# Kernel optimization log

Hardware: AMD Instinct MI355X
Metric: run time of the kernel (lower is better)

Reference implementation:

```python
import jax, jax.numpy as jnp
import numpy as np

B = 16384
D = 1024          # fusion_hidden == depth_hidden == expert hidden
ORD_H = 512       # max(48, fusion_hidden // 2)
E = 7             # num_size_classes (= number of depth experts)
C_SIZE = 7        # num_size_classes
C_DEPTH = 3       # num_depth_classes


def _lin(key, fan_in, fan_out):
    return jax.random.normal(key, (fan_in, fan_out), dtype=jnp.float32) / np.sqrt(fan_in)


def setup_inputs() -> dict:
    key = jax.random.key(0)
    ks = jax.random.split(key, 16)
    inp = {
        'hybrid_feat': jax.random.normal(ks[0], (B, D), dtype=jnp.float32),
        # size_cls_head: Linear(D, D) -> ReLU -> Linear(D, 7)
        'Wc1': _lin(ks[1], D, D), 'bc1': jnp.zeros((D,), jnp.float32),
        'Wc2': _lin(ks[2], D, C_SIZE), 'bc2': jnp.zeros((C_SIZE,), jnp.float32),
        # size_ord_head: Linear(D, 512) -> ReLU -> Linear(512, 6)
        'Wo1': _lin(ks[3], D, ORD_H), 'bo1': jnp.zeros((ORD_H,), jnp.float32),
        'Wo2': _lin(ks[4], ORD_H, C_SIZE - 1), 'bo2': jnp.zeros((C_SIZE - 1,), jnp.float32),
        # size_residual_head: Linear(D, D) -> ReLU -> Linear(D, 1)
        'Wr1': _lin(ks[5], D, D), 'br1': jnp.zeros((D,), jnp.float32),
        'Wr2': _lin(ks[6], D, 1), 'br2': jnp.zeros((1,), jnp.float32),
        # depth_adapter: Linear(D, D) -> ReLU
        'Wa': _lin(ks[7], D, D), 'ba': jnp.zeros((D,), jnp.float32),
        # 7 stacked DepthExperts: Linear(D,D) ReLU Linear(D,D) ReLU Linear(D,3)
        'We1': jax.random.normal(ks[8], (E, D, D), jnp.float32) / np.sqrt(D),
        'be1': jnp.zeros((E, D), jnp.float32),
        'We2': jax.random.normal(ks[9], (E, D, D), jnp.float32) / np.sqrt(D),
        'be2': jnp.zeros((E, D), jnp.float32),
        'We3': jax.random.normal(ks[10], (E, D, C_DEPTH), jnp.float32) / np.sqrt(D),
        'be3': jnp.zeros((E, C_DEPTH), jnp.float32),
    }
    return inp


def reference(hybrid_feat, Wc1, bc1, Wc2, bc2, Wo1, bo1, Wo2, bo2,
              Wr1, br1, Wr2, br2, Wa, ba, We1, be1, We2, be2, We3, be3):
    x = hybrid_feat  # [B, D]
    relu = jax.nn.relu
    # size classification head
    size_logits = relu(x @ Wc1 + bc1) @ Wc2 + bc2                      # [B, 7]
    # ordinal head
    size_ord_logits = relu(x @ Wo1 + bo1) @ Wo2 + bo2                  # [B, 6]
    size_probs = jax.nn.softmax(size_logits, axis=1)                   # [B, 7]
    size_values = jnp.linspace(0.0, 1.0, C_SIZE, dtype=size_probs.dtype)
    expected_norm = jnp.sum(size_probs * size_values[None, :], axis=1, keepdims=True)  # [B, 1]
    residual = 0.35 * jnp.tanh(relu(x @ Wr1 + br1) @ Wr2 + br2)        # [B, 1]
    size_reg_norm = jnp.clip(expected_norm + residual, 0.0, 1.0)       # [B, 1]
    # depth adapter + hard-routed depth experts (route_depth_logits)
    depth_feat = relu(x @ Wa + ba)                                     # [B, D]
    size_idx = jnp.argmax(size_logits, axis=1)                         # [B] hard route
    # dense all-expert compute, then per-row select == gather/scatter dispatch
    h1 = relu(jnp.einsum('bd,edh->ebh', depth_feat, We1) + be1[:, None, :])   # [E, B, D]
    h2 = relu(jnp.einsum('ebd,edh->ebh', h1, We2) + be2[:, None, :])          # [E, B, D]
    expert_logits = jnp.einsum('ebd,edc->ebc', h2, We3) + be3[:, None, :]     # [E, B, 3]
    depth_logits = jnp.take_along_axis(
        jnp.transpose(expert_logits, (1, 0, 2)),  # [B, E, 3]
        size_idx[:, None, None], axis=1)[:, 0, :]                       # [B, 3]
    # single concatenated output: [B, 7 + 6 + 1 + 7 + 3] = [B, 24]
    return jnp.concatenate(
        [size_logits, size_ord_logits, size_reg_norm, size_probs, depth_logits], axis=1)
```

## Files before the change

### kernel.cpp

```cpp
#include <hip/hip_runtime.h>
#include <cstdint>
#include <cstddef>

typedef unsigned short u16;
typedef u16 u16x8 __attribute__((ext_vector_type(8)));
typedef __bf16 bf16x8 __attribute__((ext_vector_type(8)));
typedef float f32x4 __attribute__((ext_vector_type(4)));

#define B_ROWS 16384
#define DIM 1024
#define ORDH 512
#define NEXP 7
#define NFUSE 2560

__device__ __forceinline__ u16 f2bf(float f) {
  unsigned u = __builtin_bit_cast(unsigned, f);
  u += 0x7FFFu + ((u >> 16) & 1u);
  return (u16)(u >> 16);
}
__device__ __forceinline__ float bf2f(u16 h) {
  return __builtin_bit_cast(float, ((unsigned)h) << 16);
}

typedef __attribute__((address_space(1))) const void gas_void;
typedef __attribute__((address_space(3))) void las_void;
__device__ __forceinline__ void gload16(const void* g, void* l) {
  __builtin_amdgcn_global_load_lds((gas_void*)g, (las_void*)l, 16, 0, 0);
}

__global__ void init_kernel(int* gcnt) {
  if (threadIdx.x < NEXP) gcnt[threadIdx.x] = 0;
}

__global__ __launch_bounds__(256) void convert_x_kernel(
    const float4* __restrict__ x, ushort4* __restrict__ xh,
    ushort4* __restrict__ xl) {
  const int i = blockIdx.x * 256 + threadIdx.x;
  float4 v = x[i];
  ushort4 h, l;
  h.x = f2bf(v.x); l.x = f2bf(v.x - bf2f(h.x));
  h.y = f2bf(v.y); l.y = f2bf(v.y - bf2f(h.y));
  h.z = f2bf(v.z); l.z = f2bf(v.z - bf2f(h.z));
  h.w = f2bf(v.w); l.w = f2bf(v.w - bf2f(h.w));
  xh[i] = h; xl[i] = l;
}

__global__ __launch_bounds__(256) void transpose_kernel(
    const float* __restrict__ W, u16* __restrict__ WTh, u16* __restrict__ WTl,
    int K, int N) {
  __shared__ float tile[32][33];
  const int bk = blockIdx.y * 32, bn = blockIdx.x * 32;
  const int tx = threadIdx.x & 31, ty = threadIdx.x >> 5;
  const size_t zoff = (size_t)blockIdx.z * K * N;
#pragma unroll
  for (int r = 0; r < 32; r += 8)
    tile[ty + r][tx] = W[zoff + (size_t)(bk + ty + r) * N + (bn + tx)];
  __syncthreads();
#pragma unroll
  for (int r = 0; r < 32; r += 8) {
    const float v = tile[tx][ty + r];
    const size_t o = zoff + (size_t)(bn + ty + r) * K + (bk + tx);
    const u16 h = f2bf(v);
    WTh[o] = h;
    if (WTl) WTl[o] = f2bf(v - bf2f(h));
  }
}

__device__ __forceinline__ void gemm_loop(
    const u16* __restrict__ aP0, const u16* __restrict__ bP0,
    const u16* __restrict__ aP1, const u16* __restrict__ bP1,
    const u16* __restrict__ aP2, const u16* __restrict__ bP2,
    int npass, int K, int m0, int n0, u16* SM, int tid, f32x4 (&acc)[4][4]) {
  const int lane = tid & 63;
  const int w = tid >> 6;
  const int wm = w >> 1, wn = w & 1;
  const int sRow = tid >> 3, sSlot = tid & 7;
  const int ldsOff = sRow * 64 + sSlot * 8;
  const size_t aOff = (size_t)(m0 + sRow) * K + ((sSlot ^ (sRow & 7)) * 8);
  const size_t bOff = (size_t)(n0 + sRow) * K + ((sSlot ^ (sRow & 7)) * 8);
  const u16* aCur = aP0 + aOff;
  const u16* bCur = bP0 + bOff;
  int sp = 0, sk = 0;
  auto stageNext = [&](int b) {
    u16* d = SM + b * 16384 + ldsOff;
    const u16* as = aCur + sk;
    const u16* bs = bCur + sk;
#pragma unroll
    for (int r = 0; r < 4; ++r) {
      gload16(as + (size_t)(r * 32) * K, d + r * 32 * 64);
      gload16(bs + (size_t)(r * 32) * K, d + 8192 + r * 32 * 64);
    }
    sk += 64;
    if (sk == K) {
      sk = 0; ++sp;
      if (sp == 1) { aCur = aP1 + aOff; bCur = bP1 + bOff; }
      else         { aCur = aP2 + aOff; bCur = bP2 + bOff; }
    }
  };

  const int ntiles = npass * (K >> 6);
  stageNext(0);
  int cur = 0;
  for (int ti = 0; ti < ntiles; ++ti) {
    if (ti + 1 < ntiles) {
      stageNext(cur ^ 1);
      asm volatile("s_waitcnt vmcnt(8)\n\ts_barrier" ::: "memory");
    } else {
      asm volatile("s_waitcnt vmcnt(0)\n\ts_barrier" ::: "memory");
    }
    const u16* As = SM + cur * 16384;
    const u16* Bs = As + 8192;
#pragma unroll
    for (int s = 0; s < 2; ++s) {
      const int cAx = s * 4 + (lane >> 4);
      const int colO = (cAx ^ (lane & 7)) * 8;
      bf16x8 af[4], bfr[4];
#pragma unroll
      for (int t = 0; t < 4; ++t) {
        const int rowA = wm * 64 + t * 16 + (lane & 15);
        af[t] = __builtin_bit_cast(bf16x8, *(const u16x8*)&As[rowA * 64 + colO]);
        const int rowB = wn * 64 + t * 16 + (lane & 15);
        bfr[t] = __builtin_bit_cast(bf16x8, *(const u16x8*)&Bs[rowB * 64 + colO]);
      }
#pragma unroll
      for (int mt = 0; mt < 4; ++mt)
#pragma unroll
        for (int nt = 0; nt < 4; ++nt)
          acc[mt][nt] = __builtin_amdgcn_mfma_f32_16x16x32_bf16(
              af[mt], bfr[nt], acc[mt][nt], 0, 0, 0);
    }
    asm volatile("s_barrier" ::: "memory");
    cur ^= 1;
  }
}

__global__ __launch_bounds__(256, 2) void mgemm_bt_kernel(
    const u16* __restrict__ A0, const u16* __restrict__ B0,
    const u16* __restrict__ A1, const u16* __restrict__ B1,
    const u16* __restrict__ A2, const u16* __restrict__ B2,
    int npass, int K,
    float* __restrict__ outF, const float* __restrict__ biasF, int ldoF,
    u16* __restrict__ o0, u16* __restrict__ o1, u16* __restrict__ o2,
    const float* __restrict__ b0, const float* __restrict__ b1,
    const float* __restrict__ b2) {
  __shared__ __attribute__((aligned(16))) u16 SM[4 * 128 * 64];
  const int tid = threadIdx.x;
  const int lane = tid & 63;
  const int w = tid >> 6;
  const int wm = w >> 1, wn = w & 1;
  const unsigned nwg = gridDim.x * gridDim.y;
  const unsigned wgid = blockIdx.y * gridDim.x + blockIdx.x;
  const unsigned swz = (wgid & 7u) * (nwg >> 3) + (wgid >> 3);
  const int m0 = (int)(swz / gridDim.x) * 128;
  const int n0 = (int)(swz % gridDim.x) * 128;

  f32x4 acc[4][4] = {};
  gemm_loop(A0, B0, A1, B1, A2, B2, npass, K, m0, n0, SM, tid, acc);

  const int q = lane >> 4, cl = lane & 15;
#pragma unroll
  for (int nt = 0; nt < 4; ++nt) {
    const int col = n0 + wn * 64 + nt * 16 + cl;
    if (outF) {
      const float bv = biasF[col];
#pragma unroll
      for (int mt = 0; mt < 4; ++mt)
#pragma unroll
        for (int i = 0; i < 4; ++i) {
          const int row = m0 + wm * 64 + mt * 16 + q * 4 + i;
          float v = acc[mt][nt][i] + bv;
          outF[(size_t)row * ldoF + col] = v > 0.f ? v : 0.f;
        }
    } else {
      u16* ob; const float* bp; int lc, ld;
      if (col < ORDH)            { ob = o0; bp = b0; lc = col;               ld = ORDH; }
      else if (col < ORDH + DIM) { ob = o1; bp = b1; lc = col - ORDH;        ld = DIM; }
      else                       { ob = o2; bp = b2; lc = col - (ORDH + DIM); ld = DIM; }
      const float bv = bp[lc];
#pragma unroll
      for (int mt = 0; mt < 4; ++mt)
#pragma unroll
        for (int i = 0; i < 4; ++i) {
          const int row = m0 + wm * 64 + mt * 16 + q * 4 + i;
          float v = acc[mt][nt][i] + bv;
          v = v > 0.f ? v : 0.f;
          ob[(size_t)row * ld + lc] = f2bf(v);
        }
    }
  }
}

__global__ __launch_bounds__(256, 2) void mgemm_expert_kernel(
    const u16* __restrict__ Abuf, const u16* __restrict__ Wall,
    const float* __restrict__ biasAll, const int* __restrict__ off,
    const int* __restrict__ cnt, const int* __restrict__ perm, int usePerm,
    u16* __restrict__ outH) {
  __shared__ __attribute__((aligned(16))) u16 SM[4 * 128 * 64];
  const int e = blockIdx.z;
  const int myCnt = cnt[e];
  const int t0 = blockIdx.y * 128;
  if (t0 >= myCnt) return;
  const int base = off[e];
  const int m0 = base + t0;
  const int mEnd = base + myCnt;
  const u16* Bp = Wall + (size_t)e * DIM * DIM;
  const float* bias = biasAll + (size_t)e * DIM;

  const int tid = threadIdx.x;
  const int lane = tid & 63;
  const int w = tid >> 6;
  const int wm = w >> 1, wn = w & 1;
  const int n0 = blockIdx.x * 128;
  const int sRow = tid >> 3, sSlot = tid & 7;
  const int ldsOff = sRow * 64 + sSlot * 8;
  const int swzC = (sSlot ^ (sRow & 7)) * 8;

  const u16* aSrc[4];
#pragma unroll
  for (int r = 0; r < 4; ++r) {
    int ar = m0 + r * 32 + sRow;
    if (ar > B_ROWS - 1) ar = B_ROWS - 1;
    const int gr = usePerm ? perm[ar] : ar;
    aSrc[r] = Abuf + (size_t)gr * DIM + swzC;
  }
  const u16* bSrc = Bp + (size_t)(n0 + sRow) * DIM + swzC;

  int sk = 0;
  auto stageNext = [&](int b) {
    u16* d = SM + b * 16384 + ldsOff;
#pragma unroll
    for (int r = 0; r < 4; ++r)
      gload16(aSrc[r] + sk, d + r * 32 * 64);
#pragma unroll
    for (int r = 0; r < 4; ++r)
      gload16(bSrc + (size_t)(r * 32) * DIM + sk, d + 8192 + r * 32 * 64);
    sk += 64;
  };

  f32x4 acc[4][4] = {};
  const int ntiles = DIM >> 6;
  stageNext(0);
  int cur = 0;
  for (int ti = 0; ti < ntiles; ++ti) {
    if (ti + 1 < ntiles) {
      stageNext(cur ^ 1);
      asm volatile("s_waitcnt vmcnt(8)\n\ts_barrier" ::: "memory");
    } else {
      asm volatile("s_waitcnt vmcnt(0)\n\ts_barrier" ::: "memory");
    }
    const u16* As = SM + cur * 16384;
    const u16* Bs = As + 8192;
#pragma unroll
    for (int s = 0; s < 2; ++s) {
      const int cAx = s * 4 + (lane >> 4);
      const int colO = (cAx ^ (lane & 7)) * 8;
      bf16x8 af[4], bfr[4];
#pragma unroll
      for (int t = 0; t < 4; ++t) {
        const int rowA = wm * 64 + t * 16 + (lane & 15);
        af[t] = __builtin_bit_cast(bf16x8, *(const u16x8*)&As[rowA * 64 + colO]);
        const int rowB = wn * 64 + t * 16 + (lane & 15);
        bfr[t] = __builtin_bit_cast(bf16x8, *(const u16x8*)&Bs[rowB * 64 + colO]);
      }
#pragma unroll
      for (int mt = 0; mt < 4; ++mt)
#pragma unroll
        for (int nt = 0; nt < 4; ++nt)
          acc[mt][nt] = __builtin_amdgcn_mfma_f32_16x16x32_bf16(
              af[mt], bfr[nt], acc[mt][nt], 0, 0, 0);
    }
    asm volatile("s_barrier" ::: "memory");
    cur ^= 1;
  }

  const int q = lane >> 4, cl = lane & 15;
#pragma unroll
  for (int nt = 0; nt < 4; ++nt) {
    const int col = n0 + wn * 64 + nt * 16 + cl;
    const float bv = bias[col];
#pragma unroll
    for (int mt = 0; mt < 4; ++mt) {
#pragma unroll
      for (int i = 0; i < 4; ++i) {
        const int row = m0 + wm * 64 + mt * 16 + q * 4 + i;
        if (row < mEnd) {
          float v = acc[mt][nt][i] + bv;
          v = v > 0.f ? v : 0.f;
          outH[(size_t)row * DIM + col] = f2bf(v);
        }
      }
    }
  }
}

__global__ __launch_bounds__(256) void head_res_kernel(
    const u16* __restrict__ Y3, const float* __restrict__ Wr2,
    const float* __restrict__ br2, float* __restrict__ resv) {
  const int lane = threadIdx.x & 63;
  const int r = blockIdx.x * 4 + (threadIdx.x >> 6);
  float s = 0.f;
  for (int it = 0; it < 16; ++it) {
    const int k = it * 64 + lane;
    s += bf2f(Y3[(size_t)r * DIM + k]) * Wr2[k];
  }
  for (int o = 32; o > 0; o >>= 1) s += __shfl_down(s, o);
  if (lane == 0) resv[r] = 0.35f * tanhf(s + br2[0]);
}

__global__ __launch_bounds__(256) void head_ord_kernel(
    const u16* __restrict__ Y2, const float* __restrict__ Wo2,
    const float* __restrict__ bo2, float* __restrict__ out) {
  const int lane = threadIdx.x & 63;
  const int r = blockIdx.x * 4 + (threadIdx.x >> 6);
  float s[6] = {0, 0, 0, 0, 0, 0};
  for (int it = 0; it < 8; ++it) {
    const int k = it * 64 + lane;
    const float v = bf2f(Y2[(size_t)r * ORDH + k]);
    const float* wr = Wo2 + k * 6;
#pragma unroll
    for (int n = 0; n < 6; ++n) s[n] += v * wr[n];
  }
#pragma unroll
  for (int n = 0; n < 6; ++n) {
    float xv = s[n];
    for (int o = 32; o > 0; o >>= 1) xv += __shfl_down(xv, o);
    s[n] = xv;
  }
  if (lane == 0) {
#pragma unroll
    for (int n = 0; n < 6; ++n) out[(size_t)r * 24 + 7 + n] = s[n] + bo2[n];
  }
}

__global__ __launch_bounds__(256) void head_cls_kernel(
    const float* __restrict__ Y1, const float* __restrict__ Wc2,
    const float* __restrict__ bc2, const float* __restrict__ resv,
    float* __restrict__ out, int* __restrict__ size_idx, int* __restrict__ gcnt) {
  __shared__ int lcnt[NEXP];
  const int tid = threadIdx.x;
  if (tid < NEXP) lcnt[tid] = 0;
  __syncthreads();
  const int lane = tid & 63;
  const int r = blockIdx.x * 4 + (tid >> 6);
  float s[7] = {0, 0, 0, 0, 0, 0, 0};
  for (int it = 0; it < 16; ++it) {
    const int k = it * 64 + lane;
    const float v = Y1[(size_t)r * DIM + k];
    const float* wr = Wc2 + k * 7;
#pragma unroll
    for (int n = 0; n < 7; ++n) s[n] += v * wr[n];
  }
#pragma unroll
  for (int n = 0; n < 7; ++n) {
    float xv = s[n];
    for (int o = 32; o > 0; o >>= 1) xv += __shfl_down(xv, o);
    s[n] = xv;
  }
  if (lane == 0) {
    float lg[7], p[7];
    float m = -1e30f;
    int ai = 0;
#pragma unroll
    for (int n = 0; n < 7; ++n) {
      lg[n] = s[n] + bc2[n];
      if (lg[n] > m) { m = lg[n]; ai = n; }
    }
    float es = 0.f;
#pragma unroll
    for (int n = 0; n < 7; ++n) { p[n] = expf(lg[n] - m); es += p[n]; }
    const float inv = 1.f / es;
    float expect = 0.f;
#pragma unroll
    for (int n = 0; n < 7; ++n) { p[n] *= inv; expect += p[n] * (n * (1.f / 6.f)); }
    float reg = expect + resv[r];
    reg = fminf(fmaxf(reg, 0.f), 1.f);
    float* orow = out + (size_t)r * 24;
#pragma unroll
    for (int n = 0; n < 7; ++n) orow[n] = lg[n];
    orow[13] = reg;
#pragma unroll
    for (int n = 0; n < 7; ++n) orow[14 + n] = p[n];
    size_idx[r] = ai;
    atomicAdd(&lcnt[ai], 1);
  }
  __syncthreads();
  if (tid < NEXP && lcnt[tid] > 0) atomicAdd(&gcnt[tid], lcnt[tid]);
}

__global__ void scan_kernel(const int* __restrict__ gcnt, int* __restrict__ off,
                            int* __restrict__ cursor) {
  if (threadIdx.x == 0) {
    int a = 0;
    for (int e = 0; e < NEXP; ++e) { off[e] = a; cursor[e] = a; a += gcnt[e]; }
    off[NEXP] = a;
  }
}

__global__ __launch_bounds__(256) void scatter_kernel(
    const int* __restrict__ size_idx, int* __restrict__ cursor,
    int* __restrict__ perm) {
  __shared__ int lcnt[NEXP];
  __shared__ int lbase[NEXP];
  const int tid = threadIdx.x;
  if (tid < NEXP) lcnt[tid] = 0;
  __syncthreads();
  const int r = blockIdx.x * 256 + tid;
  const int e = size_idx[r];
  const int lp = atomicAdd(&lcnt[e], 1);
  __syncthreads();
  if (tid < NEXP && lcnt[tid] > 0) lbase[tid] = atomicAdd(&cursor[tid], lcnt[tid]);
  __syncthreads();
  perm[lbase[e] + lp] = r;
}

__global__ __launch_bounds__(256) void head_dl_kernel(
    const u16* __restrict__ H2p, const float* __restrict__ We3,
    const float* __restrict__ be3, const int* __restrict__ off,
    const int* __restrict__ perm, float* __restrict__ out) {
  const int lane = threadIdx.x & 63;
  const int i = blockIdx.x * 4 + (threadIdx.x >> 6);
  int e = 0;
#pragma unroll
  for (int t = 1; t < NEXP; ++t)
    if (i >= off[t]) e = t;
  const float* W = We3 + (size_t)e * DIM * 3;
  float s0 = 0.f, s1 = 0.f, s2 = 0.f;
  for (int it = 0; it < 16; ++it) {
    const int k = it * 64 + lane;
    const float v = bf2f(H2p[(size_t)i * DIM + k]);
    s0 += v * W[k * 3 + 0];
    s1 += v * W[k * 3 + 1];
    s2 += v * W[k * 3 + 2];
  }
  for (int o = 32; o > 0; o >>= 1) {
    s0 += __shfl_down(s0, o);
    s1 += __shfl_down(s1, o);
    s2 += __shfl_down(s2, o);
  }
  if (lane == 0) {
    const int r = perm[i];
    float* orow = out + (size_t)r * 24;
    orow[21] = s0 + be3[e * 3 + 0];
    orow[22] = s1 + be3[e * 3 + 1];
    orow[23] = s2 + be3[e * 3 + 2];
  }
}

extern "C" void kernel_launch(void* const* d_in, const int* in_sizes, int n_in,
                              void* d_out, int out_size, void* d_ws, size_t ws_size,
                              hipStream_t stream) {
  (void)in_sizes; (void)n_in; (void)out_size; (void)ws_size;
  const float* x   = (const float*)d_in[0];
  const float* Wc1 = (const float*)d_in[1];
  const float* bc1 = (const float*)d_in[2];
  const float* Wc2 = (const float*)d_in[3];
  const float* bc2 = (const float*)d_in[4];
  const float* Wo1 = (const float*)d_in[5];
  const float* bo1 = (const float*)d_in[6];
  const float* Wo2 = (const float*)d_in[7];
  const float* bo2 = (const float*)d_in[8];
  const float* Wr1 = (const float*)d_in[9];
  const float* br1 = (const float*)d_in[10];
  const float* Wr2 = (const float*)d_in[11];
  const float* br2 = (const float*)d_in[12];
  const float* Wa  = (const float*)d_in[13];
  const float* ba  = (const float*)d_in[14];
  const float* We1 = (const float*)d_in[15];
  const float* be1 = (const float*)d_in[16];
  const float* We2 = (const float*)d_in[17];
  const float* be2 = (const float*)d_in[18];
  const float* We3 = (const float*)d_in[19];
  const float* be3 = (const float*)d_in[20];
  float* out = (float*)d_out;

  char* p = (char*)d_ws;
  auto carve = [&](size_t bytes) {
    char* r = p;
    p += (bytes + 255) & ~(size_t)255;
    return r;
  };
  u16* xh   = (u16*)carve((size_t)B_ROWS * DIM * 2);
  u16* xl   = (u16*)carve((size_t)B_ROWS * DIM * 2);
  u16* Tc1h = (u16*)carve((size_t)DIM * DIM * 2);
  u16* Tc1l = (u16*)carve((size_t)DIM * DIM * 2);
  u16* Tall = (u16*)carve((size_t)NFUSE * DIM * 2);
  u16* Te1  = (u16*)carve((size_t)NEXP * DIM * DIM * 2);
  u16* Te2  = (u16*)carve((size_t)NEXP * DIM * DIM * 2);
  u16* Y3   = (u16*)carve((size_t)B_ROWS * DIM * 2);
  u16* Y2   = (u16*)carve((size_t)B_ROWS * ORDH * 2);
  carve((size_t)16 << 20);
  u16* DF   = (u16*)carve((size_t)B_ROWS * DIM * 2);
  float* resv = (float*)carve((size_t)B_ROWS * 4);
  int* size_idx = (int*)carve((size_t)B_ROWS * 4);
  int* perm   = (int*)carve((size_t)B_ROWS * 4);
  int* gcnt   = (int*)carve(256);
  int* off    = (int*)carve(256);
  int* cursor = (int*)carve(256);
  float* Y1 = (float*)Y3;
  u16* H1p = Y3;
  u16* H2p = DF;
  u16* To1 = Tall;
  u16* Tr1 = Tall + (size_t)ORDH * DIM;
  u16* Ta  = Tall + (size_t)(ORDH + DIM) * DIM;

  dim3 blk(256);
  convert_x_kernel<<<dim3(B_ROWS * DIM / 4 / 256), blk, 0, stream>>>(
      (const float4*)x, (ushort4*)xh, (ushort4*)xl);
  transpose_kernel<<<dim3(32, 32, 1), blk, 0, stream>>>(Wc1, Tc1h, Tc1l, DIM, DIM);
  transpose_kernel<<<dim3(16, 32, 1), blk, 0, stream>>>(Wo1, To1, (u16*)nullptr, DIM, ORDH);
  transpose_kernel<<<dim3(32, 32, 1), blk, 0, stream>>>(Wr1, Tr1, (u16*)nullptr, DIM, DIM);
  transpose_kernel<<<dim3(32, 32, 1), blk, 0, stream>>>(Wa, Ta, (u16*)nullptr, DIM, DIM);
  transpose_kernel<<<dim3(32, 32, NEXP), blk, 0, stream>>>(We1, Te1, (u16*)nullptr, DIM, DIM);
  transpose_kernel<<<dim3(32, 32, NEXP), blk, 0, stream>>>(We2, Te2, (u16*)nullptr, DIM, DIM);
  init_kernel<<<dim3(1), dim3(64), 0, stream>>>(gcnt);

  mgemm_bt_kernel<<<dim3(NFUSE / 128, B_ROWS / 128), blk, 0, stream>>>(
      xh, Tall, xh, Tall, xh, Tall, 1, DIM,
      (float*)nullptr, (const float*)nullptr, 0,
      Y2, Y3, DF, bo1, br1, ba);
  head_res_kernel<<<dim3(B_ROWS / 4), blk, 0, stream>>>(Y3, Wr2, br2, resv);
  head_ord_kernel<<<dim3(B_ROWS / 4), blk, 0, stream>>>(Y2, Wo2, bo2, out);

  mgemm_bt_kernel<<<dim3(DIM / 128, B_ROWS / 128), blk, 0, stream>>>(
      xh, Tc1h, xh, Tc1l, xl, Tc1h, 3, DIM,
      Y1, bc1, DIM,
      (u16*)nullptr, (u16*)nullptr, (u16*)nullptr,
      (const float*)nullptr, (const float*)nullptr, (const float*)nullptr);
  head_cls_kernel<<<dim3(B_ROWS / 4), blk, 0, stream>>>(Y1, Wc2, bc2, resv, out,
                                                        size_idx, gcnt);
  scan_kernel<<<dim3(1), dim3(64), 0, stream>>>(gcnt, off, cursor);
  scatter_kernel<<<dim3(B_ROWS / 256), blk, 0, stream>>>(size_idx, cursor, perm);

  mgemm_expert_kernel<<<dim3(DIM / 128, B_ROWS / 128, NEXP), blk, 0, stream>>>(
      DF, Te1, be1, off, gcnt, perm, 1, H1p);
  mgemm_expert_kernel<<<dim3(DIM / 128, B_ROWS / 128, NEXP), blk, 0, stream>>>(
      H1p, Te2, be2, off, gcnt, perm, 0, H2p);
  head_dl_kernel<<<dim3(B_ROWS / 4), blk, 0, stream>>>(H2p, We3, be3, off, perm, out);
}
```

Before: 653.0 us.

## Halve GEMM K-tile to 32 for higher occupancy and merge small head kernels

Both GEMM kernels now stage 32-wide K tiles instead of 64, which halves LDS usage per block (32 KB down to 16 KB). They re-derive the XOR swizzle for the narrower rows and raise launch bounds from 2 to 4 blocks per CU. The intent is to hide latency through more resident waves, at the cost of twice as many barriers and loop iterations per GEMM. Separately, the gcnt init kernel is folded into convert_x, and the residual and ordinal head kernels are merged into one launch to cut launch overhead.

```diff
diff --git a/kernel.cpp b/kernel.cpp
--- a/kernel.cpp
+++ b/kernel.cpp
@@ -28,13 +28,10 @@
   __builtin_amdgcn_global_load_lds((gas_void*)g, (las_void*)l, 16, 0, 0);
 }
 
-__global__ void init_kernel(int* gcnt) {
-  if (threadIdx.x < NEXP) gcnt[threadIdx.x] = 0;
-}
-
 __global__ __launch_bounds__(256) void convert_x_kernel(
     const float4* __restrict__ x, ushort4* __restrict__ xh,
-    ushort4* __restrict__ xl) {
+    ushort4* __restrict__ xl, int* __restrict__ gcnt) {
+  if (blockIdx.x == 0 && threadIdx.x < NEXP) gcnt[threadIdx.x] = 0;
   const int i = blockIdx.x * 256 + threadIdx.x;
   float4 v = x[i];
   ushort4 h, l;
@@ -74,23 +71,24 @@
   const int lane = tid & 63;
   const int w = tid >> 6;
   const int wm = w >> 1, wn = w & 1;
-  const int sRow = tid >> 3, sSlot = tid & 7;
-  const int ldsOff = sRow * 64 + sSlot * 8;
-  const size_t aOff = (size_t)(m0 + sRow) * K + ((sSlot ^ (sRow & 7)) * 8);
-  const size_t bOff = (size_t)(n0 + sRow) * K + ((sSlot ^ (sRow & 7)) * 8);
+  const int sRow = tid >> 2, sSlot = tid & 3;
+  const int fsw = (sRow >> 1) & 3;
+  const int ldsOff = sRow * 32 + sSlot * 8;
+  const size_t aOff = (size_t)(m0 + sRow) * K + ((sSlot ^ fsw) * 8);
+  const size_t bOff = (size_t)(n0 + sRow) * K + ((sSlot ^ fsw) * 8);
   const u16* aCur = aP0 + aOff;
   const u16* bCur = bP0 + bOff;
   int sp = 0, sk = 0;
   auto stageNext = [&](int b) {
-    u16* d = SM + b * 16384 + ldsOff;
+    u16* d = SM + b * 8192 + ldsOff;
     const u16* as = aCur + sk;
     const u16* bs = bCur + sk;
 #pragma unroll
-    for (int r = 0; r < 4; ++r) {
-      gload16(as + (size_t)(r * 32) * K, d + r * 32 * 64);
-      gload16(bs + (size_t)(r * 32) * K, d + 8192 + r * 32 * 64);
-    }
-    sk += 64;
+    for (int r = 0; r < 2; ++r) {
+      gload16(as + (size_t)(r * 64) * K, d + r * 2048);
+      gload16(bs + (size_t)(r * 64) * K, d + 4096 + r * 2048);
+    }
+    sk += 32;
     if (sk == K) {
       sk = 0; ++sp;
       if (sp == 1) { aCur = aP1 + aOff; bCur = bP1 + bOff; }
@@ -98,43 +96,40 @@
     }
   };
 
-  const int ntiles = npass * (K >> 6);
+  const int ntiles = npass * (K >> 5);
   stageNext(0);
   int cur = 0;
+  const int cA = lane >> 4;
+  const int colO = (cA ^ ((lane >> 1) & 3)) * 8;
   for (int ti = 0; ti < ntiles; ++ti) {
     if (ti + 1 < ntiles) {
       stageNext(cur ^ 1);
-      asm volatile("s_waitcnt vmcnt(8)\n\ts_barrier" ::: "memory");
+      asm volatile("s_waitcnt vmcnt(4)\n\ts_barrier" ::: "memory");
     } else {
       asm volatile("s_waitcnt vmcnt(0)\n\ts_barrier" ::: "memory");
     }
-    const u16* As = SM + cur * 16384;
-    const u16* Bs = As + 8192;
-#pragma unroll
-    for (int s = 0; s < 2; ++s) {
-      const int cAx = s * 4 + (lane >> 4);
-      const int colO = (cAx ^ (lane & 7)) * 8;
-      bf16x8 af[4], bfr[4];
-#pragma unroll
-      for (int t = 0; t < 4; ++t) {
-        const int rowA = wm * 64 + t * 16 + (lane & 15);
-        af[t] = __builtin_bit_cast(bf16x8, *(const u16x8*)&As[rowA * 64 + colO]);
-        const int rowB = wn * 64 + t * 16 + (lane & 15);
-        bfr[t] = __builtin_bit_cast(bf16x8, *(const u16x8*)&Bs[rowB * 64 + colO]);
-      }
-#pragma unroll
-      for (int mt = 0; mt < 4; ++mt)
-#pragma unroll
-        for (int nt = 0; nt < 4; ++nt)
-          acc[mt][nt] = __builtin_amdgcn_mfma_f32_16x16x32_bf16(
-              af[mt], bfr[nt], acc[mt][nt], 0, 0, 0);
-    }
+    const u16* As = SM + cur * 8192;
+    const u16* Bs = As + 4096;
+    bf16x8 af[4], bfr[4];
+#pragma unroll
+    for (int t = 0; t < 4; ++t) {
+      const int rowA = wm * 64 + t * 16 + (lane & 15);
+      af[t] = __builtin_bit_cast(bf16x8, *(const u16x8*)&As[rowA * 32 + colO]);
+      const int rowB = wn * 64 + t * 16 + (lane & 15);
+      bfr[t] = __builtin_bit_cast(bf16x8, *(const u16x8*)&Bs[rowB * 32 + colO]);
+    }
+#pragma unroll
+    for (int mt = 0; mt < 4; ++mt)
+#pragma unroll
+      for (int nt = 0; nt < 4; ++nt)
+        acc[mt][nt] = __builtin_amdgcn_mfma_f32_16x16x32_bf16(
+            af[mt], bfr[nt], acc[mt][nt], 0, 0, 0);
     asm volatile("s_barrier" ::: "memory");
     cur ^= 1;
   }
 }
 
-__global__ __launch_bounds__(256, 2) void mgemm_bt_kernel(
+__global__ __launch_bounds__(256, 4) void mgemm_bt_kernel(
     const u16* __restrict__ A0, const u16* __restrict__ B0,
     const u16* __restrict__ A1, const u16* __restrict__ B1,
     const u16* __restrict__ A2, const u16* __restrict__ B2,
@@ -143,7 +138,7 @@
     u16* __restrict__ o0, u16* __restrict__ o1, u16* __restrict__ o2,
     const float* __restrict__ b0, const float* __restrict__ b1,
     const float* __restrict__ b2) {
-  __shared__ __attribute__((aligned(16))) u16 SM[4 * 128 * 64];
+  __shared__ __attribute__((aligned(16))) u16 SM[2 * 8192];
   const int tid = threadIdx.x;
   const int lane = tid & 63;
   const int w = tid >> 6;
@@ -190,12 +185,12 @@
   }
 }
 
-__global__ __launch_bounds__(256, 2) void mgemm_expert_kernel(
+__global__ __launch_bounds__(256, 4) void mgemm_expert_kernel(
     const u16* __restrict__ Abuf, const u16* __restrict__ Wall,
     const float* __restrict__ biasAll, const int* __restrict__ off,
     const int* __restrict__ cnt, const int* __restrict__ perm, int usePerm,
     u16* __restrict__ outH) {
-  __shared__ __attribute__((aligned(16))) u16 SM[4 * 128 * 64];
+  __shared__ __attribute__((aligned(16))) u16 SM[2 * 8192];
   const int e = blockIdx.z;
   const int myCnt = cnt[e];
   const int t0 = blockIdx.y * 128;
@@ -211,14 +206,15 @@
   const int w = tid >> 6;
   const int wm = w >> 1, wn = w & 1;
   const int n0 = blockIdx.x * 128;
-  const int sRow = tid >> 3, sSlot = tid & 7;
-  const int ldsOff = sRow * 64 + sSlot * 8;
-  const int swzC = (sSlot ^ (sRow & 7)) * 8;
-
-  const u16* aSrc[4];
-#pragma unroll
-  for (int r = 0; r < 4; ++r) {
-    int ar = m0 + r * 32 + sRow;
+  const int sRow = tid >> 2, sSlot = tid & 3;
+  const int fsw = (sRow >> 1) & 3;
+  const int ldsOff = sRow * 32 + sSlot * 8;
+  const int swzC = (sSlot ^ fsw) * 8;
+
+  const u16* aSrc[2];
+#pragma unroll
+  for (int r = 0; r < 2; ++r) {
+    int ar = m0 + r * 64 + sRow;
     if (ar > B_ROWS - 1) ar = B_ROWS - 1;
     const int gr = usePerm ? perm[ar] : ar;
     aSrc[r] = Abuf + (size_t)gr * DIM + swzC;
@@ -227,48 +223,44 @@
 
   int sk = 0;
   auto stageNext = [&](int b) {
-    u16* d = SM + b * 16384 + ldsOff;
-#pragma unroll
-    for (int r = 0; r < 4; ++r)
-      gload16(aSrc[r] + sk, d + r * 32 * 64);
-#pragma unroll
-    for (int r = 0; r < 4; ++r)
-      gload16(bSrc + (size_t)(r * 32) * DIM + sk, d + 8192 + r * 32 * 64);
-    sk += 64;
+    u16* d = SM + b * 8192 + ldsOff;
+#pragma unroll
+    for (int r = 0; r < 2; ++r) {
+      gload16(aSrc[r] + sk, d + r * 2048);
+      gload16(bSrc + (size_t)(r * 64) * DIM + sk, d + 4096 + r * 2048);
+    }
+    sk += 32;
   };
 
   f32x4 acc[4][4] = {};
-  const int ntiles = DIM >> 6;
+  const int ntiles = DIM >> 5;
   stageNext(0);
   int cur = 0;
+  const int cA = lane >> 4;
+  const int colO = (cA ^ ((lane >> 1) & 3)) * 8;
   for (int ti = 0; ti < ntiles; ++ti) {
     if (ti + 1 < ntiles) {
       stageNext(cur ^ 1);
-      asm volatile("s_waitcnt vmcnt(8)\n\ts_barrier" ::: "memory");
+      asm volatile("s_waitcnt vmcnt(4)\n\ts_barrier" ::: "memory");
     } else {
       asm volatile("s_waitcnt vmcnt(0)\n\ts_barrier" ::: "memory");
     }
-    const u16* As = SM + cur * 16384;
-    const u16* Bs = As + 8192;
-#pragma unroll
-    for (int s = 0; s < 2; ++s) {
-      const int cAx = s * 4 + (lane >> 4);
-      const int colO = (cAx ^ (lane & 7)) * 8;
-      bf16x8 af[4], bfr[4];
-#pragma unroll
-      for (int t = 0; t < 4; ++t) {
-        const int rowA = wm * 64 + t * 16 + (lane & 15);
-        af[t] = __builtin_bit_cast(bf16x8, *(const u16x8*)&As[rowA * 64 + colO]);
-        const int rowB = wn * 64 + t * 16 + (lane & 15);
-        bfr[t] = __builtin_bit_cast(bf16x8, *(const u16x8*)&Bs[rowB * 64 + colO]);
-      }
-#pragma unroll
-      for (int mt = 0; mt < 4; ++mt)
-#pragma unroll
-        for (int nt = 0; nt < 4; ++nt)
-          acc[mt][nt] = __builtin_amdgcn_mfma_f32_16x16x32_bf16(
-              af[mt], bfr[nt], acc[mt][nt], 0, 0, 0);
-    }
+    const u16* As = SM + cur * 8192;
+    const u16* Bs = As + 4096;
+    bf16x8 af[4], bfr[4];
+#pragma unroll
+    for (int t = 0; t < 4; ++t) {
+      const int rowA = wm * 64 + t * 16 + (lane & 15);
+      af[t] = __builtin_bit_cast(bf16x8, *(const u16x8*)&As[rowA * 32 + colO]);
+      const int rowB = wn * 64 + t * 16 + (lane & 15);
+      bfr[t] = __builtin_bit_cast(bf16x8, *(const u16x8*)&Bs[rowB * 32 + colO]);
+    }
+#pragma unroll
+    for (int mt = 0; mt < 4; ++mt)
+#pragma unroll
+      for (int nt = 0; nt < 4; ++nt)
+        acc[mt][nt] = __builtin_amdgcn_mfma_f32_16x16x32_bf16(
+            af[mt], bfr[nt], acc[mt][nt], 0, 0, 0);
     asm volatile("s_barrier" ::: "memory");
     cur ^= 1;
   }
@@ -293,9 +285,11 @@
   }
 }
 
-__global__ __launch_bounds__(256) void head_res_kernel(
+__global__ __launch_bounds__(256) void head_resord_kernel(
     const u16* __restrict__ Y3, const float* __restrict__ Wr2,
-    const float* __restrict__ br2, float* __restrict__ resv) {
+    const float* __restrict__ br2, float* __restrict__ resv,
+    const u16* __restrict__ Y2, const float* __restrict__ Wo2,
+    const float* __restrict__ bo2, float* __restrict__ out) {
   const int lane = threadIdx.x & 63;
   const int r = blockIdx.x * 4 + (threadIdx.x >> 6);
   float s = 0.f;
@@ -305,30 +299,23 @@
   }
   for (int o = 32; o > 0; o >>= 1) s += __shfl_down(s, o);
   if (lane == 0) resv[r] = 0.35f * tanhf(s + br2[0]);
-}
-
-__global__ __launch_bounds__(256) void head_ord_kernel(
-    const u16* __restrict__ Y2, const float* __restrict__ Wo2,
-    const float* __restrict__ bo2, float* __restrict__ out) {
-  const int lane = threadIdx.x & 63;
-  const int r = blockIdx.x * 4 + (threadIdx.x >> 6);
-  float s[6] = {0, 0, 0, 0, 0, 0};
+  float so[6] = {0, 0, 0, 0, 0, 0};
   for (int it = 0; it < 8; ++it) {
     const int k = it * 64 + lane;
     const float v = bf2f(Y2[(size_t)r * ORDH + k]);
     const float* wr = Wo2 + k * 6;
 #pragma unroll
-    for (int n = 0; n < 6; ++n) s[n] += v * wr[n];
+    for (int n = 0; n < 6; ++n) so[n] += v * wr[n];
   }
 #pragma unroll
   for (int n = 0; n < 6; ++n) {
-    float xv = s[n];
+    float xv = so[n];
     for (int o = 32; o > 0; o >>= 1) xv += __shfl_down(xv, o);
-    s[n] = xv;
+    so[n] = xv;
   }
   if (lane == 0) {
 #pragma unroll
-    for (int n = 0; n < 6; ++n) out[(size_t)r * 24 + 7 + n] = s[n] + bo2[n];
+    for (int n = 0; n < 6; ++n) out[(size_t)r * 24 + 7 + n] = so[n] + bo2[n];
   }
 }
 
@@ -505,21 +492,20 @@
 
   dim3 blk(256);
   convert_x_kernel<<<dim3(B_ROWS * DIM / 4 / 256), blk, 0, stream>>>(
-      (const float4*)x, (ushort4*)xh, (ushort4*)xl);
+      (const float4*)x, (ushort4*)xh, (ushort4*)xl, gcnt);
   transpose_kernel<<<dim3(32, 32, 1), blk, 0, stream>>>(Wc1, Tc1h, Tc1l, DIM, DIM);
   transpose_kernel<<<dim3(16, 32, 1), blk, 0, stream>>>(Wo1, To1, (u16*)nullptr, DIM, ORDH);
   transpose_kernel<<<dim3(32, 32, 1), blk, 0, stream>>>(Wr1, Tr1, (u16*)nullptr, DIM, DIM);
   transpose_kernel<<<dim3(32, 32, 1), blk, 0, stream>>>(Wa, Ta, (u16*)nullptr, DIM, DIM);
   transpose_kernel<<<dim3(32, 32, NEXP), blk, 0, stream>>>(We1, Te1, (u16*)nullptr, DIM, DIM);
   transpose_kernel<<<dim3(32, 32, NEXP), blk, 0, stream>>>(We2, Te2, (u16*)nullptr, DIM, DIM);
-  init_kernel<<<dim3(1), dim3(64), 0, stream>>>(gcnt);
 
   mgemm_bt_kernel<<<dim3(NFUSE / 128, B_ROWS / 128), blk, 0, stream>>>(
       xh, Tall, xh, Tall, xh, Tall, 1, DIM,
       (float*)nullptr, (const float*)nullptr, 0,
       Y2, Y3, DF, bo1, br1, ba);
-  head_res_kernel<<<dim3(B_ROWS / 4), blk, 0, stream>>>(Y3, Wr2, br2, resv);
-  head_ord_kernel<<<dim3(B_ROWS / 4), blk, 0, stream>>>(Y2, Wo2, bo2, out);
+  head_resord_kernel<<<dim3(B_ROWS / 4), blk, 0, stream>>>(
+      Y3, Wr2, br2, resv, Y2, Wo2, bo2, out);
 
   mgemm_bt_kernel<<<dim3(DIM / 128, B_ROWS / 128), blk, 0, stream>>>(
       xh, Tc1h, xh, Tc1l, xl, Tc1h, 3, DIM,
```

Measured after the change: 681.7 us. +4.4%, slower.
